# Kernel tuning notes

Measured on AMD Instinct MI355X. Metric: run time of the kernel, lower is better.

The kernel has to match this reference:

```python
import jax, jax.numpy as jnp
import numpy as np

T, B, D, H = 2048, 128, 128, 256

def setup_inputs() -> dict:
    key = jax.random.key(0)
    k1, k2, k3, k4, k5, k6 = jax.random.split(key, 6)
    s_in = 1.0 / np.sqrt(D)
    s_h = 1.0 / np.sqrt(H)
    return {
        "x": jax.random.normal(k1, (T, B, D), dtype=jnp.float32),
        "h": jnp.zeros((B, H), dtype=jnp.float32),
        "W_in": jax.random.uniform(k2, (D, H), jnp.float32, -s_in, s_in),
        "b_in": jax.random.uniform(k3, (H,), jnp.float32, -s_in, s_in),
        "W_h": jax.random.uniform(k4, (H, H), jnp.float32, -s_h, s_h),
        "b_h": jax.random.uniform(k5, (H,), jnp.float32, -s_h, s_h),
    }

def reference(x, h, W_in, b_in, W_h, b_h):
    # Precompute input projections for all timesteps in one big GEMM:
    # [T,B,D] @ [D,H] -> [T,B,H]
    xproj = jnp.einsum('tbd,dh->tbh', x, W_in) + b_in + b_h

    def step(h, xp_t):
        h_next = jnp.tanh(xp_t + h @ W_h)
        return h_next, h_next

    _, h_seq = jax.lax.scan(step, h, xproj)
    return h_seq  # [T, B, H]
```

## Files before the change

### kernel.cpp

```cpp
#include <hip/hip_runtime.h>

#define TT 2048
#define BB 128
#define DD 128
#define HH 256

typedef float f32x4 __attribute__((ext_vector_type(4)));
typedef _Float16 f16x8 __attribute__((ext_vector_type(8)));
typedef _Float16 f16x4 __attribute__((ext_vector_type(4)));

static __device__ __forceinline__ float fast_tanh(float s) {
    float e = __expf(2.0f * s);
    float r = __builtin_amdgcn_rcpf(e + 1.0f);
    return __builtin_fmaf(-2.0f, r, 1.0f);
}

static __device__ __forceinline__ void lds_barrier() {
    __builtin_amdgcn_sched_barrier(0);
    asm volatile("s_waitcnt lgkmcnt(0)" ::: "memory");
    __builtin_amdgcn_s_barrier();
    __builtin_amdgcn_sched_barrier(0);
}

__global__ __launch_bounds__(256, 2) void xproj_mfma(
    const float* __restrict__ x, const float* __restrict__ W_in,
    const float* __restrict__ b_in, const float* __restrict__ b_h,
    float* __restrict__ out)
{
    __shared__ short xs[64 * 128];
    const int tid  = threadIdx.x;
    const int lane = tid & 63;
    const int w    = tid >> 6;
    const int lrow = lane & 15;
    const int lgrp = lane >> 4;
    const long rbase = (long)blockIdx.x * 64;

    f16x8 bw[4][4];
    #pragma unroll
    for (int kc = 0; kc < 4; ++kc)
        #pragma unroll
        for (int nt = 0; nt < 4; ++nt) {
            const int n = w * 64 + nt * 16 + lrow;
            #pragma unroll
            for (int i = 0; i < 8; ++i)
                bw[kc][nt][i] = (_Float16)W_in[(kc * 32 + lgrp * 8 + i) * HH + n];
        }
    float bias[4];
    #pragma unroll
    for (int nt = 0; nt < 4; ++nt) {
        const int n = w * 64 + nt * 16 + lrow;
        bias[nt] = b_in[n] + b_h[n];
    }

    {
        const float4* xg = (const float4*)(x + rbase * DD);
        #pragma unroll
        for (int th = 0; th < 8; ++th) {
            int idx = tid + th * 256;
            int r   = idx >> 5;
            int c4  = idx & 31;
            float4 v = xg[idx];
            f16x4 p;
            p[0] = (_Float16)v.x; p[1] = (_Float16)v.y;
            p[2] = (_Float16)v.z; p[3] = (_Float16)v.w;
            unsigned off = (unsigned)(r * 256 + c4 * 8);
            off ^= (unsigned)((r & 7) << 4);
            *(f16x4*)((char*)xs + off) = p;
        }
    }
    __syncthreads();

    #pragma unroll
    for (int mt = 0; mt < 4; ++mt) {
        const int r = mt * 16 + lrow;
        f16x8 a[4];
        #pragma unroll
        for (int kc = 0; kc < 4; ++kc) {
            unsigned off = (unsigned)(r * 256 + kc * 64 + lgrp * 16);
            off ^= (unsigned)((r & 7) << 4);
            a[kc] = *(const f16x8*)((const char*)xs + off);
        }
        f32x4 acc[4];
        #pragma unroll
        for (int nt = 0; nt < 4; ++nt) { f32x4 c = {bias[nt], bias[nt], bias[nt], bias[nt]}; acc[nt] = c; }
        #pragma unroll
        for (int kc = 0; kc < 4; ++kc)
            #pragma unroll
            for (int nt = 0; nt < 4; ++nt)
                acc[nt] = __builtin_amdgcn_mfma_f32_16x16x32_f16(a[kc], bw[kc][nt], acc[nt], 0, 0, 0);
        #pragma unroll
        for (int nt = 0; nt < 4; ++nt)
            #pragma unroll
            for (int rr = 0; rr < 4; ++rr)
                out[(rbase + mt * 16 + lgrp * 4 + rr) * HH + w * 64 + nt * 16 + lrow] = acc[nt][rr];
    }
}

struct RecCtx {
    float* io;
    int b0, lrow, lgrp, jb;
};

static __device__ __forceinline__ void rec_step(
    const RecCtx& c, int t,
    f32x4 (&xp)[2],
    const short* curb, short* nxtb,
    const f16x8 (&wh)[2][8])
{
    f32x4 xpn[2];
    const int t2 = (t + 2 < TT) ? t + 2 : TT - 1;
    #pragma unroll
    for (int mt = 0; mt < 2; ++mt)
        xpn[mt] = *(const f32x4*)(c.io + ((long)t2 * BB + c.b0 + c.lrow) * HH + c.jb + mt * 16 + c.lgrp * 4);

    f16x8 bbf[8];
    #pragma unroll
    for (int kc = 0; kc < 8; ++kc) {
        unsigned off = (unsigned)(c.lrow * 512 + kc * 64 + c.lgrp * 16);
        off ^= (unsigned)((c.lrow & 7) << 4);
        bbf[kc] = *(const f16x8*)((const char*)curb + off);
    }

    f32x4 accA[2], accB[2];
    #pragma unroll
    for (int mt = 0; mt < 2; ++mt) {
        accA[mt] = xp[mt];
        f32x4 z = {0.f, 0.f, 0.f, 0.f};
        accB[mt] = z;
        xp[mt] = xpn[mt];
    }

    __builtin_amdgcn_s_setprio(1);
    #pragma unroll
    for (int kc = 0; kc < 4; ++kc)
        #pragma unroll
        for (int mt = 0; mt < 2; ++mt) {
            accA[mt] = __builtin_amdgcn_mfma_f32_16x16x32_f16(wh[mt][kc],     bbf[kc],     accA[mt], 0, 0, 0);
            accB[mt] = __builtin_amdgcn_mfma_f32_16x16x32_f16(wh[mt][kc + 4], bbf[kc + 4], accB[mt], 0, 0, 0);
        }
    __builtin_amdgcn_s_setprio(0);

    #pragma unroll
    for (int mt = 0; mt < 2; ++mt) {
        f32x4 s4 = accA[mt] + accB[mt];
        f32x4 hv;
        #pragma unroll
        for (int rr = 0; rr < 4; ++rr) hv[rr] = fast_tanh(s4[rr]);
        *(f32x4*)(c.io + ((long)t * BB + c.b0 + c.lrow) * HH + c.jb + mt * 16 + c.lgrp * 4) = hv;
        f16x4 q;
        #pragma unroll
        for (int rr = 0; rr < 4; ++rr) q[rr] = (_Float16)hv[rr];
        unsigned off = (unsigned)(c.lrow * 512 + (c.jb + mt * 16 + c.lgrp * 4) * 2);
        off ^= (unsigned)((c.lrow & 7) << 4);
        *(f16x4*)((char*)nxtb + off) = q;
    }
    lds_barrier();
}

__global__ __launch_bounds__(512, 2) void rnn_rec_mfma(
    const float* __restrict__ h0, const float* __restrict__ W_h,
    float* io)
{
    __shared__ short hb0[16 * 256];
    __shared__ short hb1[16 * 256];
    const int tid  = threadIdx.x;
    const int lane = tid & 63;
    const int w    = tid >> 6;
    const int lrow = lane & 15;
    const int lgrp = lane >> 4;
    const int b0   = blockIdx.x * 16;
    const int jb   = w * 32;

    f16x8 wh[2][8];
    #pragma unroll
    for (int mt = 0; mt < 2; ++mt) {
        const int j = jb + mt * 16 + lrow;
        #pragma unroll
        for (int kc = 0; kc < 8; ++kc)
            #pragma unroll
            for (int i = 0; i < 8; ++i)
                wh[mt][kc][i] = (_Float16)W_h[(kc * 32 + lgrp * 8 + i) * HH + j];
    }

    {
        const int g  = tid >> 5;
        const int k0 = (tid & 31) * 8;
        const float* hp = h0 + (b0 + g) * HH + k0;
        f16x8 p;
        #pragma unroll
        for (int i = 0; i < 8; ++i) p[i] = (_Float16)hp[i];
        unsigned off = (unsigned)(g * 512 + k0 * 2);
        off ^= (unsigned)((g & 7) << 4);
        *(f16x8*)((char*)hb0 + off) = p;
    }

    RecCtx c{io, b0, lrow, lgrp, jb};

    f32x4 xa[2], xb[2];
    #pragma unroll
    for (int mt = 0; mt < 2; ++mt) {
        xa[mt] = *(const f32x4*)(io + ((long)0 * BB + b0 + lrow) * HH + jb + mt * 16 + lgrp * 4);
        xb[mt] = *(const f32x4*)(io + ((long)1 * BB + b0 + lrow) * HH + jb + mt * 16 + lgrp * 4);
    }

    __syncthreads();

    for (int t = 0; t < TT; t += 2) {
        rec_step(c, t,     xa, hb0, hb1, wh);
        rec_step(c, t + 1, xb, hb1, hb0, wh);
    }
}

extern "C" void kernel_launch(void* const* d_in, const int* in_sizes, int n_in,
                              void* d_out, int out_size, void* d_ws, size_t ws_size,
                              hipStream_t stream) {
    const float* x    = (const float*)d_in[0];
    const float* h0   = (const float*)d_in[1];
    const float* W_in = (const float*)d_in[2];
    const float* b_in = (const float*)d_in[3];
    const float* W_h  = (const float*)d_in[4];
    const float* b_h  = (const float*)d_in[5];
    float* out = (float*)d_out;

    xproj_mfma<<<(TT * BB) / 64, 256, 0, stream>>>(x, W_in, b_in, b_h, out);
    rnn_rec_mfma<<<BB / 16, 512, 0, stream>>>(h0, W_h, out);
}
```

Before: 2.060 ms.

## Process two batch tiles per block sharing one barrier per timestep

The recurrence kernel now handles two independent 16-row batch tiles per block, with separate double-buffered LDS hidden states. It issues both tiles' MFMA chains before a single barrier and defers the output stores until after the barrier. The intent is to amortize barrier latency and let independent MFMA and tanh work overlap on the serial critical path. In exchange, half as many blocks run and each step does twice the work per wave, so latency per step may grow.

```diff
diff --git a/kernel.cpp b/kernel.cpp
--- a/kernel.cpp
+++ b/kernel.cpp
@@ -96,79 +96,114 @@
     }
 }
 
-struct RecCtx {
-    float* io;
-    int b0, lrow, lgrp, jb;
-};
-
-static __device__ __forceinline__ void rec_step(
-    const RecCtx& c, int t,
-    f32x4 (&xp)[2],
-    const short* curb, short* nxtb,
+template<bool PF>
+static __device__ __forceinline__ void rec_period(
+    float* io, int p, int b0A, int b0B, int lrow, int lgrp, int jb,
+    f32x4 (&xqA)[2], f32x4 (&xqB)[2],
+    const short* curA, short* nxtA, const short* curB, short* nxtB,
     const f16x8 (&wh)[2][8])
 {
-    f32x4 xpn[2];
-    const int t2 = (t + 2 < TT) ? t + 2 : TT - 1;
-    #pragma unroll
-    for (int mt = 0; mt < 2; ++mt)
-        xpn[mt] = *(const f32x4*)(c.io + ((long)t2 * BB + c.b0 + c.lrow) * HH + c.jb + mt * 16 + c.lgrp * 4);
-
-    f16x8 bbf[8];
-    #pragma unroll
-    for (int kc = 0; kc < 8; ++kc) {
-        unsigned off = (unsigned)(c.lrow * 512 + kc * 64 + c.lgrp * 16);
-        off ^= (unsigned)((c.lrow & 7) << 4);
-        bbf[kc] = *(const f16x8*)((const char*)curb + off);
-    }
-
-    f32x4 accA[2], accB[2];
+    f32x4 hvA[2], hvB[2];
+
+    {
+        f16x8 bbf[8];
+        #pragma unroll
+        for (int kc = 0; kc < 8; ++kc) {
+            unsigned off = (unsigned)(lrow * 512 + kc * 64 + lgrp * 16) ^ (unsigned)((lrow & 7) << 4);
+            bbf[kc] = *(const f16x8*)((const char*)curA + off);
+        }
+        f32x4 acc0[2], acc1[2];
+        #pragma unroll
+        for (int mt = 0; mt < 2; ++mt) {
+            acc0[mt] = xqA[mt];
+            f32x4 z = {0.f, 0.f, 0.f, 0.f};
+            acc1[mt] = z;
+        }
+        if (PF) {
+            #pragma unroll
+            for (int mt = 0; mt < 2; ++mt)
+                xqA[mt] = *(const f32x4*)(io + ((long)(p + 2) * BB + b0A + lrow) * HH + jb + mt * 16 + lgrp * 4);
+        }
+        #pragma unroll
+        for (int kc = 0; kc < 4; ++kc)
+            #pragma unroll
+            for (int mt = 0; mt < 2; ++mt) {
+                acc0[mt] = __builtin_amdgcn_mfma_f32_16x16x32_f16(wh[mt][kc],     bbf[kc],     acc0[mt], 0, 0, 0);
+                acc1[mt] = __builtin_amdgcn_mfma_f32_16x16x32_f16(wh[mt][kc + 4], bbf[kc + 4], acc1[mt], 0, 0, 0);
+            }
+        #pragma unroll
+        for (int mt = 0; mt < 2; ++mt) {
+            f32x4 s4 = acc0[mt] + acc1[mt];
+            #pragma unroll
+            for (int rr = 0; rr < 4; ++rr) hvA[mt][rr] = fast_tanh(s4[rr]);
+            f16x4 q;
+            #pragma unroll
+            for (int rr = 0; rr < 4; ++rr) q[rr] = (_Float16)hvA[mt][rr];
+            unsigned off = (unsigned)(lrow * 512 + (jb + mt * 16 + lgrp * 4) * 2) ^ (unsigned)((lrow & 7) << 4);
+            *(f16x4*)((char*)nxtA + off) = q;
+        }
+    }
+    {
+        f16x8 bbf[8];
+        #pragma unroll
+        for (int kc = 0; kc < 8; ++kc) {
+            unsigned off = (unsigned)(lrow * 512 + kc * 64 + lgrp * 16) ^ (unsigned)((lrow & 7) << 4);
+            bbf[kc] = *(const f16x8*)((const char*)curB + off);
+        }
+        f32x4 acc0[2], acc1[2];
+        #pragma unroll
+        for (int mt = 0; mt < 2; ++mt) {
+            acc0[mt] = xqB[mt];
+            f32x4 z = {0.f, 0.f, 0.f, 0.f};
+            acc1[mt] = z;
+        }
+        if (PF) {
+            #pragma unroll
+            for (int mt = 0; mt < 2; ++mt)
+                xqB[mt] = *(const f32x4*)(io + ((long)(p + 2) * BB + b0B + lrow) * HH + jb + mt * 16 + lgrp * 4);
+        }
+        #pragma unroll
+        for (int kc = 0; kc < 4; ++kc)
+            #pragma unroll
+            for (int mt = 0; mt < 2; ++mt) {
+                acc0[mt] = __builtin_amdgcn_mfma_f32_16x16x32_f16(wh[mt][kc],     bbf[kc],     acc0[mt], 0, 0, 0);
+                acc1[mt] = __builtin_amdgcn_mfma_f32_16x16x32_f16(wh[mt][kc + 4], bbf[kc + 4], acc1[mt], 0, 0, 0);
+            }
+        #pragma unroll
+        for (int mt = 0; mt < 2; ++mt) {
+            f32x4 s4 = acc0[mt] + acc1[mt];
+            #pragma unroll
+            for (int rr = 0; rr < 4; ++rr) hvB[mt][rr] = fast_tanh(s4[rr]);
+            f16x4 q;
+            #pragma unroll
+            for (int rr = 0; rr < 4; ++rr) q[rr] = (_Float16)hvB[mt][rr];
+            unsigned off = (unsigned)(lrow * 512 + (jb + mt * 16 + lgrp * 4) * 2) ^ (unsigned)((lrow & 7) << 4);
+            *(f16x4*)((char*)nxtB + off) = q;
+        }
+    }
+
+    lds_barrier();
+
     #pragma unroll
     for (int mt = 0; mt < 2; ++mt) {
-        accA[mt] = xp[mt];
-        f32x4 z = {0.f, 0.f, 0.f, 0.f};
-        accB[mt] = z;
-        xp[mt] = xpn[mt];
-    }
-
-    __builtin_amdgcn_s_setprio(1);
-    #pragma unroll
-    for (int kc = 0; kc < 4; ++kc)
-        #pragma unroll
-        for (int mt = 0; mt < 2; ++mt) {
-            accA[mt] = __builtin_amdgcn_mfma_f32_16x16x32_f16(wh[mt][kc],     bbf[kc],     accA[mt], 0, 0, 0);
-            accB[mt] = __builtin_amdgcn_mfma_f32_16x16x32_f16(wh[mt][kc + 4], bbf[kc + 4], accB[mt], 0, 0, 0);
-        }
-    __builtin_amdgcn_s_setprio(0);
-
-    #pragma unroll
-    for (int mt = 0; mt < 2; ++mt) {
-        f32x4 s4 = accA[mt] + accB[mt];
-        f32x4 hv;
-        #pragma unroll
-        for (int rr = 0; rr < 4; ++rr) hv[rr] = fast_tanh(s4[rr]);
-        *(f32x4*)(c.io + ((long)t * BB + c.b0 + c.lrow) * HH + c.jb + mt * 16 + c.lgrp * 4) = hv;
-        f16x4 q;
-        #pragma unroll
-        for (int rr = 0; rr < 4; ++rr) q[rr] = (_Float16)hv[rr];
-        unsigned off = (unsigned)(c.lrow * 512 + (c.jb + mt * 16 + c.lgrp * 4) * 2);
-        off ^= (unsigned)((c.lrow & 7) << 4);
-        *(f16x4*)((char*)nxtb + off) = q;
-    }
-    lds_barrier();
+        *(f32x4*)(io + ((long)p * BB + b0A + lrow) * HH + jb + mt * 16 + lgrp * 4) = hvA[mt];
+        *(f32x4*)(io + ((long)p * BB + b0B + lrow) * HH + jb + mt * 16 + lgrp * 4) = hvB[mt];
+    }
 }
 
 __global__ __launch_bounds__(512, 2) void rnn_rec_mfma(
     const float* __restrict__ h0, const float* __restrict__ W_h,
     float* io)
 {
-    __shared__ short hb0[16 * 256];
-    __shared__ short hb1[16 * 256];
+    __shared__ short hA0[16 * 256], hA1[16 * 256];
+    __shared__ short hB0[16 * 256], hB1[16 * 256];
     const int tid  = threadIdx.x;
     const int lane = tid & 63;
     const int w    = tid >> 6;
     const int lrow = lane & 15;
     const int lgrp = lane >> 4;
-    const int b0   = blockIdx.x * 16;
+    const int b0A  = blockIdx.x * 32;
+    const int b0B  = b0A + 16;
     const int jb   = w * 32;
 
     f16x8 wh[2][8];
@@ -183,32 +218,39 @@
     }
 
     {
-        const int g  = tid >> 5;
-        const int k0 = (tid & 31) * 8;
-        const float* hp = h0 + (b0 + g) * HH + k0;
-        f16x8 p;
-        #pragma unroll
-        for (int i = 0; i < 8; ++i) p[i] = (_Float16)hp[i];
-        unsigned off = (unsigned)(g * 512 + k0 * 2);
-        off ^= (unsigned)((g & 7) << 4);
-        *(f16x8*)((char*)hb0 + off) = p;
-    }
-
-    RecCtx c{io, b0, lrow, lgrp, jb};
-
-    f32x4 xa[2], xb[2];
+        const int g  = tid >> 4;
+        const int k0 = (tid & 15) * 16;
+        const float* hp = h0 + (b0A + g) * HH + k0;
+        f16x8 p0, p1;
+        #pragma unroll
+        for (int i = 0; i < 8; ++i) { p0[i] = (_Float16)hp[i]; p1[i] = (_Float16)hp[8 + i]; }
+        short* buf = (g < 16) ? hA0 : hB0;
+        const int gl = g & 15;
+        unsigned off0 = (unsigned)(gl * 512 + k0 * 2)      ^ (unsigned)((gl & 7) << 4);
+        unsigned off1 = (unsigned)(gl * 512 + k0 * 2 + 16) ^ (unsigned)((gl & 7) << 4);
+        *(f16x8*)((char*)buf + off0) = p0;
+        *(f16x8*)((char*)buf + off1) = p1;
+    }
+
+    f32x4 xqA0[2], xqA1[2], xqB0[2], xqB1[2];
     #pragma unroll
     for (int mt = 0; mt < 2; ++mt) {
-        xa[mt] = *(const f32x4*)(io + ((long)0 * BB + b0 + lrow) * HH + jb + mt * 16 + lgrp * 4);
-        xb[mt] = *(const f32x4*)(io + ((long)1 * BB + b0 + lrow) * HH + jb + mt * 16 + lgrp * 4);
+        const long o = (long)(b0A + lrow) * HH + jb + mt * 16 + lgrp * 4;
+        const long oB = (long)(b0B + lrow) * HH + jb + mt * 16 + lgrp * 4;
+        xqA0[mt] = *(const f32x4*)(io + (long)0 * BB * HH + o);
+        xqA1[mt] = *(const f32x4*)(io + (long)1 * BB * HH + o);
+        xqB0[mt] = *(const f32x4*)(io + (long)0 * BB * HH + oB);
+        xqB1[mt] = *(const f32x4*)(io + (long)1 * BB * HH + oB);
     }
 
     __syncthreads();
 
-    for (int t = 0; t < TT; t += 2) {
-        rec_step(c, t,     xa, hb0, hb1, wh);
-        rec_step(c, t + 1, xb, hb1, hb0, wh);
-    }
+    for (int p = 0; p < TT - 2; p += 2) {
+        rec_period<true>(io, p,     b0A, b0B, lrow, lgrp, jb, xqA0, xqB0, hA0, hA1, hB0, hB1, wh);
+        rec_period<true>(io, p + 1, b0A, b0B, lrow, lgrp, jb, xqA1, xqB1, hA1, hA0, hB1, hB0, wh);
+    }
+    rec_period<false>(io, TT - 2, b0A, b0B, lrow, lgrp, jb, xqA0, xqB0, hA0, hA1, hB0, hB1, wh);
+    rec_period<false>(io, TT - 1, b0A, b0B, lrow, lgrp, jb, xqA1, xqB1, hA1, hA0, hB1, hB0, wh);
 }
 
 extern "C" void kernel_launch(void* const* d_in, const int* in_sizes, int n_in,
@@ -223,5 +265,5 @@
     float* out = (float*)d_out;
 
     xproj_mfma<<<(TT * BB) / 64, 256, 0, stream>>>(x, W_in, b_in, b_h, out);
-    rnn_rec_mfma<<<BB / 16, 512, 0, stream>>>(h0, W_h, out);
-}
+    rnn_rec_mfma<<<BB / 32, 512, 0, stream>>>(h0, W_h, out);
+}
```

New measurement: 3.938 ms. 1.91x slower.
